# Optimization experiments

Hardware: AMD Instinct MI355X
Metric: run time of the kernel (lower is better)

Reference implementation:

```python
import jax, jax.numpy as jnp
import numpy as np

B, T, S = 4, 16384, 256
V_DIM, L_DIM, E, H = 256, 768, 1024, 8
D = E // H  # head_dim = 128
SCALE = D ** -0.5
CLAMP = 50000.0


def setup_inputs() -> dict:
    key = jax.random.key(0)
    ks = jax.random.split(key, 8)
    w = lambda k, shp: jax.random.normal(k, shp, jnp.float32) * 0.03  # ~xavier scale
    return {
        'v': jax.random.normal(ks[0], (B, T, V_DIM), jnp.float32),
        'l': jax.random.normal(ks[1], (B, S, L_DIM), jnp.float32),
        'v_proj_w': w(ks[2], (V_DIM, E)), 'v_proj_b': jnp.zeros((E,), jnp.float32),
        'l_proj_w': w(ks[3], (L_DIM, E)), 'l_proj_b': jnp.zeros((E,), jnp.float32),
        'vv_w': w(ks[4], (V_DIM, E)), 'vv_b': jnp.zeros((E,), jnp.float32),
        'vl_w': w(ks[5], (L_DIM, E)), 'vl_b': jnp.zeros((E,), jnp.float32),
        'ov_w': w(ks[6], (E, V_DIM)), 'ov_b': jnp.zeros((V_DIM,), jnp.float32),
        'ol_w': w(ks[7], (E, L_DIM)), 'ol_b': jnp.zeros((L_DIM,), jnp.float32),
    }


def _heads(x):
    # [B, N, E] -> [B, H, N, D]
    b, n, _ = x.shape
    return x.reshape(b, n, H, D).transpose(0, 2, 1, 3)


def reference(v, l, v_proj_w, v_proj_b, l_proj_w, l_proj_b,
              vv_w, vv_b, vl_w, vl_b, ov_w, ov_b, ol_w, ol_b):
    b, t, _ = v.shape
    s = l.shape[1]
    q = _heads((v @ v_proj_w + v_proj_b) * SCALE)   # [B,H,T,D]
    k = _heads(l @ l_proj_w + l_proj_b)             # [B,H,S,D]
    val_v = _heads(v @ vv_w + vv_b)                 # [B,H,T,D]
    val_l = _heads(l @ vl_w + vl_b)                 # [B,H,S,D]

    attn = jnp.einsum('bhtd,bhsd->bhts', q, k)      # shared QK^T scores
    attn = jnp.clip(attn, -CLAMP, CLAMP)

    # column-direction softmax (over vision tokens) on the transpose
    attn_T = attn.transpose(0, 1, 3, 2)             # [B,H,S,T]
    attn_l = attn_T - jnp.max(attn_T, axis=-1, keepdims=True)
    attn_l = jnp.clip(attn_l, -CLAMP, CLAMP)
    attn_l = jax.nn.softmax(attn_l, axis=-1)

    # row-direction softmax (over text tokens)
    attn_v = jax.nn.softmax(attn, axis=-1)          # [B,H,T,S]

    out_v = jnp.einsum('bhts,bhsd->bhtd', attn_v, val_l)
    out_l = jnp.einsum('bhst,bhtd->bhsd', attn_l, val_v)
    out_v = out_v.transpose(0, 2, 1, 3).reshape(b, t, E)
    out_l = out_l.transpose(0, 2, 1, 3).reshape(b, s, E)
    return out_v @ ov_w + ov_b, out_l @ ol_w + ol_b
```

## Files before the change

kernel.cpp:

```cpp
#include <hip/hip_runtime.h>
#include <hip/hip_bf16.h>
#include <hip/hip_fp16.h>

#define DI __device__ __forceinline__

typedef short bf16x8 __attribute__((ext_vector_type(8)));
typedef float f32x4 __attribute__((ext_vector_type(4)));
using bf16 = __hip_bfloat16;

typedef __attribute__((address_space(3))) void lds_void;
typedef const __attribute__((address_space(1))) void glob_void;

constexpr int Tn = 16384, Sn = 256, En = 1024;
constexpr float SCALEF = 0.08838834764831845f;
constexpr float CLAMPF = 50000.0f;

DI f32x4 mfma16(bf16x8 a, bf16x8 b, f32x4 c) {
  return __builtin_amdgcn_mfma_f32_16x16x32_bf16(a, b, c, 0, 0, 0);
}
DI unsigned short f2bu(float x) { bf16 h = __float2bfloat16(x); return *(unsigned short*)&h; }
DI unsigned int pack2(float lo, float hi) { return (unsigned)f2bu(lo) | ((unsigned)f2bu(hi) << 16); }
DI bf16x8 ldg8(const bf16* p) { return *(const bf16x8*)p; }
DI float clampf(float v) { return fminf(fmaxf(v, -CLAMPF), CLAMPF); }
DI unsigned int packh2(float a, float b) {
  __half2 h = __floats2half2_rn(a, b);
  return *(unsigned int*)&h;
}
DI void gload16(const bf16* g, bf16* lds_base) {
  __builtin_amdgcn_global_load_lds((glob_void*)g, (lds_void*)lds_base, 16, 0, 0);
}

__global__ void cast_f32_bf16_v4(const float* __restrict__ in, bf16* __restrict__ out, int n4) {
  int i = blockIdx.x * 256 + threadIdx.x;
  if (i >= n4) return;
  float4 f = reinterpret_cast<const float4*>(in)[i];
  unsigned long long u = (unsigned long long)pack2(f.x, f.y) |
                         ((unsigned long long)pack2(f.z, f.w) << 32);
  *reinterpret_cast<unsigned long long*>(out + (size_t)i * 4) = u;
}

__global__ void cast_weights(const float* __restrict__ w0, bf16* __restrict__ o0,
                             const float* __restrict__ w1, bf16* __restrict__ o1,
                             const float* __restrict__ w2, bf16* __restrict__ o2,
                             const float* __restrict__ w3, bf16* __restrict__ o3,
                             const float* __restrict__ w4, bf16* __restrict__ o4,
                             const float* __restrict__ w5, bf16* __restrict__ o5) {
  int id = blockIdx.x * 256 + threadIdx.x;
  switch (blockIdx.y) {
    case 0: if (id < 256*1024) { int k = id >> 10, n = id & 1023; o0[n*256 + k] = __float2bfloat16(w0[id]); } break;
    case 1: if (id < 256*1024) { int k = id >> 10, n = id & 1023; o1[n*256 + k] = __float2bfloat16(w1[id]); } break;
    case 2: if (id < 768*1024) { int k = id >> 10, n = id & 1023; o2[n*768 + k] = __float2bfloat16(w2[id]); } break;
    case 3: if (id < 768*1024) { int k = id >> 10, n = id & 1023; o3[n*768 + k] = __float2bfloat16(w3[id]); } break;
    case 4: if (id < 1024*256) { int k = id >> 8,  n = id & 255;  o4[n*1024 + k] = __float2bfloat16(w4[id]); } break;
    case 5: if (id < 1024*768) { int k = id / 768, n = id % 768;  o5[n*1024 + k] = __float2bfloat16(w5[id]); } break;
  }
}

template<int MODE>
__global__ __launch_bounds__(256) void gemm_kern(
    const bf16* __restrict__ A, const bf16* __restrict__ Bw0, const bf16* __restrict__ Bw1,
    const float* __restrict__ bias0, const float* __restrict__ bias1,
    void* __restrict__ out0, void* __restrict__ out1, int zbase)
{
  constexpr int K = (MODE == 0) ? 256 : (MODE == 1) ? 768 : 1024;
  const int z = blockIdx.z + zbase;
  const bf16* Bw = z ? Bw1 : Bw0;
  const float* bias = z ? bias1 : bias0;
  const int m0 = blockIdx.x * 128, n0 = blockIdx.y * 128;
  const int tid = threadIdx.x, lane = tid & 63;
  const int w = tid >> 6, wm = w >> 1, wn = w & 1;
  const int l15 = lane & 15, l4 = lane >> 4;

  __shared__ bf16 smem[128 * 136];
  bf16* As = smem;
  bf16* Bs = smem + 128 * 64;

  const int lr = lane >> 3, lp = lane & 7;

  f32x4 acc[4][4];
  #pragma unroll
  for (int a = 0; a < 4; a++)
    #pragma unroll
    for (int c = 0; c < 4; c++) acc[a][c] = f32x4{0.f, 0.f, 0.f, 0.f};

  for (int k0 = 0; k0 < K; k0 += 64) {
    __syncthreads();
    #pragma unroll
    for (int it = 0; it < 4; it++) {
      const int row = it * 32 + w * 8 + lr;
      const int gc = lp ^ (row & 7);
      gload16(Bw + (size_t)(n0 + row) * K + k0 + gc * 8, Bs + (it * 32 + w * 8) * 64);
      gload16(A  + (size_t)(m0 + row) * K + k0 + gc * 8, As + (it * 32 + w * 8) * 64);
    }
    __syncthreads();
    #pragma unroll
    for (int ks = 0; ks < 2; ks++) {
      bf16x8 af[4], bfr[4];
      #pragma unroll
      for (int mf = 0; mf < 4; mf++) {
        int r = wm * 64 + mf * 16 + l15;
        af[mf] = *(const bf16x8*)(As + r * 64 + (((ks * 4 + l4) ^ (r & 7)) * 8));
      }
      #pragma unroll
      for (int nf = 0; nf < 4; nf++) {
        int r = wn * 64 + nf * 16 + l15;
        bfr[nf] = *(const bf16x8*)(Bs + r * 64 + (((ks * 4 + l4) ^ (r & 7)) * 8));
      }
      #pragma unroll
      for (int mf = 0; mf < 4; mf++)
        #pragma unroll
        for (int nf = 0; nf < 4; nf++)
          acc[mf][nf] = mfma16(af[mf], bfr[nf], acc[mf][nf]);
    }
  }
  __syncthreads();

  if constexpr (MODE <= 1) {
    #pragma unroll
    for (int nf = 0; nf < 4; nf++) {
      int nl = wn * 64 + nf * 16 + l15;
      float bv = bias[n0 + nl];
      #pragma unroll
      for (int mf = 0; mf < 4; mf++) {
        int ml = wm * 64 + mf * 16 + l4 * 4;
        #pragma unroll
        for (int i = 0; i < 4; i++) {
          float vv = acc[mf][nf][i] + bv;
          if (MODE == 0 && z == 0) vv *= SCALEF;
          smem[(ml + i) * 136 + nl] = __float2bfloat16(vv);
        }
      }
    }
    __syncthreads();
    constexpr int TT = (MODE == 0) ? Tn : Sn;
    const int h = n0 >> 7;
    const int r2 = tid >> 1, c0 = (tid & 1) * 64;
    if (z == 0) {
      int m = m0 + r2;
      int bq = (MODE == 0) ? 0 : (m >> 8);
      int t  = m & (TT - 1);
      bf16* out = (bf16*)out0;
      size_t base = ((size_t)(bq * 8 + h) * TT + t) * 128 + c0;
      #pragma unroll
      for (int j = 0; j < 32; j++) {
        unsigned int u = *(const unsigned int*)(smem + r2 * 136 + c0 + 2 * j);
        *(unsigned int*)(out + base + 2 * j) = u;
      }
    } else {
      int bq = (MODE == 0) ? 0 : (m0 >> 8);
      int t0 = m0 & (TT - 1);
      bf16* out = (bf16*)out1;
      size_t base = ((size_t)(bq * 8 + h) * 128 + r2) * TT + t0 + c0;
      #pragma unroll
      for (int j = 0; j < 32; j++) {
        unsigned short u0 = *(const unsigned short*)(smem + (c0 + 2 * j)     * 136 + r2);
        unsigned short u1 = *(const unsigned short*)(smem + (c0 + 2 * j + 1) * 136 + r2);
        *(unsigned int*)(out + base + 2 * j) = (unsigned)u0 | ((unsigned)u1 << 16);
      }
    }
  } else {
    constexpr int NOUT = (MODE == 2) ? 256 : 768;
    float* out = (float*)out0;
    #pragma unroll
    for (int nf = 0; nf < 4; nf++) {
      int n = n0 + wn * 64 + nf * 16 + l15;
      float bv = bias[n];
      #pragma unroll
      for (int mf = 0; mf < 4; mf++) {
        size_t mbase = (size_t)(m0 + wm * 64 + mf * 16 + l4 * 4) * NOUT + n;
        #pragma unroll
        for (int i = 0; i < 4; i++)
          out[mbase + (size_t)i * NOUT] = acc[mf][nf][i] + bv;
      }
    }
  }
}

template<int NCH, bool SLAB>
__global__ __launch_bounds__(512, 2) void attn_fused(
    const bf16* __restrict__ qh,
    const bf16* __restrict__ kh,
    const bf16* __restrict__ vallT,
    const bf16* __restrict__ valvT,
    bf16* __restrict__ ovh,
    void* __restrict__ col_dst,
    float* __restrict__ dsum_dst)
{
  constexpr int SPAN = Tn / NCH;
  constexpr int TILES = SPAN / 64;
  const int ch = blockIdx.x, h = blockIdx.y;
  const int tid = threadIdx.x, lane = tid & 63, w = tid >> 6;
  const int l15 = lane & 15, l4 = lane >> 4;
  const int sw = w * 32;
  const int e7 = l15 & 7;

  __shared__ bf16 Qb[2][64 * 128];
  __shared__ bf16 Vb[2][128 * 64];
  __shared__ bf16 Enat[64 * 264];
  __shared__ bf16 Etr[8][32 * 72];
  __shared__ float red[8][64];

  const bf16* qp  = qh    + (size_t)h * Tn * 128;
  const bf16* kp  = kh    + (size_t)h * Sn * 128;
  const bf16* vlp = vallT + (size_t)h * 128 * Sn;
  const bf16* vvp = valvT + (size_t)h * 128 * Tn;
  const int tb0 = ch * SPAN;

  bf16x8 bkr[4][2];
  #pragma unroll
  for (int ks = 0; ks < 4; ks++)
    #pragma unroll
    for (int si = 0; si < 2; si++)
      bkr[ks][si] = ldg8(kp + (size_t)(sw + si * 16 + l15) * 128 + ks * 32 + l4 * 8);
  bf16x8 bvr[8];
  #pragma unroll
  for (int ks2 = 0; ks2 < 8; ks2++)
    bvr[ks2] = ldg8(vlp + (size_t)(w * 16 + l15) * Sn + ks2 * 32 + l4 * 8);

  const int q_r0 = tid >> 4, q_c = tid & 15;
  const int q_r1 = q_r0 + 32;
  const int v_r0 = tid >> 3, v_c = tid & 7;
  const int v_r1 = v_r0 + 64;

  {
    uint4 q0 = *(const uint4*)(qp + (size_t)(tb0 + q_r0) * 128 + q_c * 8);
    uint4 q1 = *(const uint4*)(qp + (size_t)(tb0 + q_r1) * 128 + q_c * 8);
    uint4 v0 = *(const uint4*)(vvp + (size_t)v_r0 * Tn + tb0 + v_c * 8);
    uint4 v1 = *(const uint4*)(vvp + (size_t)v_r1 * Tn + tb0 + v_c * 8);
    *(uint4*)(&Qb[0][q_r0 * 128 + ((q_c ^ (q_r0 & 7)) * 8)]) = q0;
    *(uint4*)(&Qb[0][q_r1 * 128 + ((q_c ^ (q_r1 & 7)) * 8)]) = q1;
    *(uint4*)(&Vb[0][v_r0 * 64  + ((v_c ^ (v_r0 & 7)) * 8)]) = v0;
    *(uint4*)(&Vb[0][v_r1 * 64  + ((v_c ^ (v_r1 & 7)) * 8)]) = v1;
  }
  __syncthreads();

  f32x4 oc[8][2];
  #pragma unroll
  for (int a = 0; a < 8; a++)
    #pragma unroll
    for (int c = 0; c < 2; c++) oc[a][c] = f32x4{0.f, 0.f, 0.f, 0.f};
  float csum[2] = {0.f, 0.f};

  int cur = 0;
  for (int tt = 0; tt < TILES; tt++) {
    const int tb = tb0 + tt * 64;
    const bool hn = (tt + 1 < TILES);
    uint4 pfq0, pfq1, pfv0, pfv1;
    if (hn) {
      const int tbn = tb + 64;
      pfq0 = *(const uint4*)(qp + (size_t)(tbn + q_r0) * 128 + q_c * 8);
      pfq1 = *(const uint4*)(qp + (size_t)(tbn + q_r1) * 128 + q_c * 8);
      pfv0 = *(const uint4*)(vvp + (size_t)v_r0 * Tn + tbn + v_c * 8);
      pfv1 = *(const uint4*)(vvp + (size_t)v_r1 * Tn + tbn + v_c * 8);
    }
    f32x4 sacc[4][2];
    #pragma unroll
    for (int a = 0; a < 4; a++)
      #pragma unroll
      for (int c = 0; c < 2; c++) sacc[a][c] = f32x4{0.f, 0.f, 0.f, 0.f};
    #pragma unroll
    for (int ks = 0; ks < 4; ks++) {
      const int x = (ks * 4 + l4) ^ e7;
      bf16x8 aq[4];
      #pragma unroll
      for (int ti = 0; ti < 4; ti++)
        aq[ti] = *(const bf16x8*)(&Qb[cur][(ti * 16 + l15) * 128 + x * 8]);
      #pragma unroll
      for (int ti = 0; ti < 4; ti++)
        #pragma unroll
        for (int si = 0; si < 2; si++)
          sacc[ti][si] = mfma16(aq[ti], bkr[ks][si], sacc[ti][si]);
    }
    float rp[4][4];
    #pragma unroll
    for (int ti = 0; ti < 4; ti++)
      #pragma unroll
      for (int i = 0; i < 4; i++) rp[ti][i] = 0.f;
    #pragma unroll
    for (int ti = 0; ti < 4; ti++)
      #pragma unroll
      for (int si = 0; si < 2; si++) {
        float e0 = __expf(clampf(sacc[ti][si][0]));
        float e1 = __expf(clampf(sacc[ti][si][1]));
        float e2 = __expf(clampf(sacc[ti][si][2]));
        float e3 = __expf(clampf(sacc[ti][si][3]));
        csum[si] += (e0 + e1) + (e2 + e3);
        rp[ti][0] += e0; rp[ti][1] += e1; rp[ti][2] += e2; rp[ti][3] += e3;
        unsigned long long u = (unsigned long long)pack2(e0, e1) |
                               ((unsigned long long)pack2(e2, e3) << 32);
        *(unsigned long long*)(&Etr[w][(si * 16 + l15) * 72 + ti * 16 + l4 * 4]) = u;
        const int s = sw + si * 16 + l15;
        const int t0 = ti * 16 + l4 * 4;
        Enat[(t0 + 0) * 264 + s] = __float2bfloat16(e0);
        Enat[(t0 + 1) * 264 + s] = __float2bfloat16(e1);
        Enat[(t0 + 2) * 264 + s] = __float2bfloat16(e2);
        Enat[(t0 + 3) * 264 + s] = __float2bfloat16(e3);
      }
    #pragma unroll
    for (int ti = 0; ti < 4; ti++)
      #pragma unroll
      for (int i = 0; i < 4; i++) {
        float r = rp[ti][i];
        #pragma unroll
        for (int off = 1; off < 16; off <<= 1) r += __shfl_xor(r, off);
        if (l15 == 0) red[w][ti * 16 + l4 * 4 + i] = r;
      }
    __syncthreads();
    float rsm[4][4];
    #pragma unroll
    for (int ti = 0; ti < 4; ti++)
      #pragma unroll
      for (int i = 0; i < 4; i++) {
        const int tl = ti * 16 + l4 * 4 + i;
        float s = red[0][tl] + red[1][tl] + red[2][tl] + red[3][tl] +
                  red[4][tl] + red[5][tl] + red[6][tl] + red[7][tl];
        rsm[ti][i] = 1.0f / s;
      }
    f32x4 orr[4];
    #pragma unroll
    for (int a = 0; a < 4; a++) orr[a] = f32x4{0.f, 0.f, 0.f, 0.f};
    #pragma unroll
    for (int ks2 = 0; ks2 < 8; ks2++) {
      const int soff = ks2 * 32 + l4 * 8;
      #pragma unroll
      for (int ti = 0; ti < 4; ti++) {
        bf16x8 ap = *(const bf16x8*)(Enat + (ti * 16 + l15) * 264 + soff);
        orr[ti] = mfma16(ap, bvr[ks2], orr[ti]);
      }
    }
    #pragma unroll
    for (int ti = 0; ti < 4; ti++) {
      size_t base = (size_t)(tb + ti * 16 + l4 * 4) * En + h * 128 + w * 16 + l15;
      #pragma unroll
      for (int i = 0; i < 4; i++)
        ovh[base + (size_t)i * En] = __float2bfloat16(orr[ti][i] * rsm[ti][i]);
    }
    #pragma unroll
    for (int kst = 0; kst < 2; kst++) {
      bf16x8 bp[2];
      #pragma unroll
      for (int si = 0; si < 2; si++)
        bp[si] = *(const bf16x8*)(&Etr[w][(si * 16 + l15) * 72 + kst * 32 + l4 * 8]);
      const int x = (kst * 4 + l4) ^ e7;
      #pragma unroll
      for (int mf = 0; mf < 8; mf++) {
        bf16x8 av = *(const bf16x8*)(&Vb[cur][(mf * 16 + l15) * 64 + x * 8]);
        #pragma unroll
        for (int si = 0; si < 2; si++)
          oc[mf][si] = mfma16(av, bp[si], oc[mf][si]);
      }
    }
    if (hn) {
      *(uint4*)(&Qb[cur ^ 1][q_r0 * 128 + ((q_c ^ (q_r0 & 7)) * 8)]) = pfq0;
      *(uint4*)(&Qb[cur ^ 1][q_r1 * 128 + ((q_c ^ (q_r1 & 7)) * 8)]) = pfq1;
      *(uint4*)(&Vb[cur ^ 1][v_r0 * 64  + ((v_c ^ (v_r0 & 7)) * 8)]) = pfv0;
      *(uint4*)(&Vb[cur ^ 1][v_r1 * 64  + ((v_c ^ (v_r1 & 7)) * 8)]) = pfv1;
    }
    __syncthreads();
    cur ^= 1;
  }
  #pragma unroll
  for (int si = 0; si < 2; si++) {
    float c = csum[si];
    c += __shfl_xor(c, 16);
    c += __shfl_xor(c, 32);
    if (l4 == 0) {
      if constexpr (SLAB) dsum_dst[((size_t)(ch * 8 + h)) * 256 + sw + si * 16 + l15] = c;
      else atomicAdd(&dsum_dst[h * 256 + sw + si * 16 + l15], c);
    }
  }
  if constexpr (SLAB) {
    __half* slab = (__half*)col_dst + ((size_t)(ch * 8 + h) * 256) * 128;
    #pragma unroll
    for (int mf = 0; mf < 8; mf++)
      #pragma unroll
      for (int si = 0; si < 2; si++) {
        const int s = sw + si * 16 + l15;
        const int d = mf * 16 + l4 * 4;
        uint2 u;
        u.x = packh2(oc[mf][si][0], oc[mf][si][1]);
        u.y = packh2(oc[mf][si][2], oc[mf][si][3]);
        *(uint2*)(slab + (size_t)s * 128 + d) = u;
      }
  } else {
    float* olh = (float*)col_dst;
    #pragma unroll
    for (int mf = 0; mf < 8; mf++)
      #pragma unroll
      for (int si = 0; si < 2; si++) {
        const int s = sw + si * 16 + l15;
        const int d = mf * 16 + l4 * 4;
        float* dst = olh + (size_t)s * 1024 + h * 128 + d;
        #pragma unroll
        for (int i = 0; i < 4; i++) atomicAdd(dst + i, oc[mf][si][i]);
      }
  }
}

template<int NCH>
__global__ __launch_bounds__(256) void reduce_olh(
    const __half* __restrict__ slab, const float* __restrict__ csum_slab, bf16* __restrict__ olhb)
{
  int id = blockIdx.x * 256 + threadIdx.x;
  int s = id >> 8, hd4 = id & 255, h = hd4 >> 5, d4 = hd4 & 31;
  float a0 = 0.f, a1 = 0.f, a2 = 0.f, a3 = 0.f, dsv = 0.f;
  #pragma unroll 4
  for (int ch = 0; ch < NCH; ch++) {
    uint2 u = *(const uint2*)(slab + ((size_t)(ch * 8 + h) * 256 + s) * 128 + d4 * 4);
    __half2 x = *(__half2*)&u.x, y = *(__half2*)&u.y;
    a0 += __low2float(x); a1 += __high2float(x);
    a2 += __low2float(y); a3 += __high2float(y);
    dsv += csum_slab[((size_t)(ch * 8 + h)) * 256 + s];
  }
  float inv = 1.0f / dsv;
  unsigned long long u = (unsigned long long)pack2(a0 * inv, a1 * inv) |
                         ((unsigned long long)pack2(a2 * inv, a3 * inv) << 32);
  *reinterpret_cast<unsigned long long*>(olhb + (size_t)s * 1024 + h * 128 + d4 * 4) = u;
}

__global__ __launch_bounds__(256) void norm_olh(
    const float* __restrict__ olh, const float* __restrict__ dsum, bf16* __restrict__ olhb)
{
  int i = blockIdx.x * 256 + threadIdx.x;
  int s = i >> 8, c4 = i & 255;
  float inv = 1.0f / dsum[(c4 >> 5) * 256 + s];
  float4 x = reinterpret_cast<const float4*>(olh + (size_t)s * 1024)[c4];
  unsigned long long u = (unsigned long long)pack2(x.x * inv, x.y * inv) |
                         ((unsigned long long)pack2(x.z * inv, x.w * inv) << 32);
  *reinterpret_cast<unsigned long long*>(olhb + (size_t)s * 1024 + c4 * 4) = u;
}

extern "C" void kernel_launch(void* const* d_in, const int* in_sizes, int n_in,
                              void* d_out, int out_size, void* d_ws, size_t ws_size,
                              hipStream_t stream)
{
  (void)in_sizes; (void)n_in;
  const float* v        = (const float*)d_in[0];
  const float* l        = (const float*)d_in[1];
  const float* v_proj_w = (const float*)d_in[2];
  const float* v_proj_b = (const float*)d_in[3];
  const float* l_proj_w = (const float*)d_in[4];
  const float* l_proj_b = (const float*)d_in[5];
  const float* vv_w     = (const float*)d_in[6];
  const float* vv_b     = (const float*)d_in[7];
  const float* vl_w     = (const float*)d_in[8];
  const float* vl_b     = (const float*)d_in[9];
  const float* ov_w     = (const float*)d_in[10];
  const float* ov_b     = (const float*)d_in[11];
  const float* ol_w     = (const float*)d_in[12];
  const float* ol_b     = (const float*)d_in[13];

  char* ws = (char*)d_ws;
  size_t off = 0;
  auto alloc = [&](size_t bytes) -> char* {
    char* p = ws + off;
    off += (bytes + 255) & ~(size_t)255;
    return p;
  };

  bf16*  wqt   = (bf16*)alloc((size_t)1024 * 256 * 2);
  bf16*  wvvt  = (bf16*)alloc((size_t)1024 * 256 * 2);
  bf16*  wkt   = (bf16*)alloc((size_t)1024 * 768 * 2);
  bf16*  wvlt  = (bf16*)alloc((size_t)1024 * 768 * 2);
  bf16*  wovt  = (bf16*)alloc((size_t)256 * 1024 * 2);
  bf16*  wolt  = (bf16*)alloc((size_t)768 * 1024 * 2);
  bf16*  lb    = (bf16*)alloc((size_t)1024 * 768 * 2);
  bf16*  kh    = (bf16*)alloc((size_t)32 * 256 * 128 * 2);
  bf16*  vallT = (bf16*)alloc((size_t)32 * 128 * 256 * 2);
  float* olh   = (float*)alloc((size_t)1024 * 1024 * 4);
  bf16*  olhb  = (bf16*)alloc((size_t)1024 * 1024 * 2);
  float* dsum  = (float*)alloc((size_t)2048 * 4);
  bf16*  vb_b    = (bf16*)alloc((size_t)16384 * 256 * 2);
  bf16*  qh_b    = (bf16*)alloc((size_t)8 * 16384 * 128 * 2);
  bf16*  valvT_b = (bf16*)alloc((size_t)8 * 128 * 16384 * 2);
  bf16*  ovh_b   = (bf16*)alloc((size_t)16384 * 1024 * 2);
  const size_t off_base = off;

  const size_t slabh_b = (size_t)32 * 8 * 256 * 128 * 2;
  const size_t csum_b  = (size_t)32 * 8 * 256 * 4;
  int tier;
  if (off_base + slabh_b + csum_b <= ws_size) tier = 0;
  else if (off_base <= ws_size) tier = 2;
  else {
    hipMemsetAsync(d_out, 0xFF, (size_t)out_size * 4, stream);
    return;
  }
  __half* slabh     = (__half*)(ws + off_base);
  float*  csum_slab = (float*)(ws + off_base + slabh_b);

  if (tier == 2) hipMemsetAsync(olh, 0, (size_t)1024 * 1024 * 4, stream);

  cast_weights<<<dim3(3072, 6), 256, 0, stream>>>(v_proj_w, wqt, vv_w, wvvt,
                                                  l_proj_w, wkt, vl_w, wvlt, ov_w, wovt, ol_w, wolt);
  cast_f32_bf16_v4<<<768, 256, 0, stream>>>(l, lb, 196608);
  gemm_kern<1><<<dim3(8, 8, 2), 256, 0, stream>>>(lb, wkt, wvlt, l_proj_b, vl_b, kh, vallT, 0);

  for (int b = 0; b < 4; b++) {
    const bf16*  kh_b    = kh    + (size_t)b * 8 * Sn * 128;
    const bf16*  vallT_b = vallT + (size_t)b * 8 * 128 * Sn;
    cast_f32_bf16_v4<<<4096, 256, 0, stream>>>(v + (size_t)b * 16384 * 256, vb_b, 1048576);
    gemm_kern<0><<<dim3(128, 8, 2), 256, 0, stream>>>(vb_b, wqt, wvvt, v_proj_b, vv_b,
                                                      qh_b, valvT_b, 0);
    if (tier == 0) {
      attn_fused<32, true><<<dim3(32, 8), 512, 0, stream>>>(qh_b, kh_b, vallT_b, valvT_b,
                                                            ovh_b, slabh, csum_slab);
    } else {
      hipMemsetAsync(dsum, 0, (size_t)2048 * 4, stream);
      attn_fused<32, false><<<dim3(32, 8), 512, 0, stream>>>(qh_b, kh_b, vallT_b, valvT_b,
                                                             ovh_b, olh + (size_t)b * 256 * 1024, dsum);
    }
    gemm_kern<2><<<dim3(128, 2, 1), 256, 0, stream>>>(ovh_b, wovt, wovt, ov_b, ov_b,
                                                      (float*)d_out + (size_t)b * 16384 * 256, nullptr, 0);
    if (tier == 0) reduce_olh<32><<<256, 256, 0, stream>>>(slabh, csum_slab, olhb + (size_t)b * 256 * 1024);
    else           norm_olh<<<256, 256, 0, stream>>>(olh + (size_t)b * 256 * 1024, dsum,
                                                     olhb + (size_t)b * 256 * 1024);
  }

  gemm_kern<3><<<dim3(8, 6, 1), 256, 0, stream>>>(olhb, wolt, wolt, ol_b, ol_b,
                                                  (float*)d_out + 16777216, nullptr, 0);
}
```

Before: 646.0 us.

## Stage out_v tile through LDS for coalesced stores and raise MFMA priority

The per-tile attention output for the vision stream is written to a swizzled shared-memory buffer. It is then stored to global memory one iteration later as 16-byte coalesced vectors, replacing the scattered 2-byte stores. MFMA sections are wrapped in s_setprio to favor matrix-issuing waves, and the symmetric score clamp is replaced by a one-sided cap before exp. This adds 16KB of LDS per block, which may reduce occupancy, and the deferred store relies on the existing end-of-loop barrier for correctness.

New measurement: 731.2 us. 1.13x slower.

```diff
diff --git a/kernel.cpp b/kernel.cpp
--- a/kernel.cpp
+++ b/kernel.cpp
@@ -13,7 +13,7 @@
 
 constexpr int Tn = 16384, Sn = 256, En = 1024;
 constexpr float SCALEF = 0.08838834764831845f;
-constexpr float CLAMPF = 50000.0f;
+constexpr float EXPCAP = 80.0f;
 
 DI f32x4 mfma16(bf16x8 a, bf16x8 b, f32x4 c) {
   return __builtin_amdgcn_mfma_f32_16x16x32_bf16(a, b, c, 0, 0, 0);
@@ -21,7 +21,6 @@
 DI unsigned short f2bu(float x) { bf16 h = __float2bfloat16(x); return *(unsigned short*)&h; }
 DI unsigned int pack2(float lo, float hi) { return (unsigned)f2bu(lo) | ((unsigned)f2bu(hi) << 16); }
 DI bf16x8 ldg8(const bf16* p) { return *(const bf16x8*)p; }
-DI float clampf(float v) { return fminf(fmaxf(v, -CLAMPF), CLAMPF); }
 DI unsigned int packh2(float a, float b) {
   __half2 h = __floats2half2_rn(a, b);
   return *(unsigned int*)&h;
@@ -198,6 +197,7 @@
   __shared__ bf16 Vb[2][128 * 64];
   __shared__ bf16 Enat[64 * 264];
   __shared__ bf16 Etr[8][32 * 72];
+  __shared__ bf16 Ob[64 * 128];
   __shared__ float red[8][64];
 
   const bf16* qp  = qh    + (size_t)h * Tn * 128;
@@ -221,6 +221,8 @@
   const int q_r1 = q_r0 + 32;
   const int v_r0 = tid >> 3, v_c = tid & 7;
   const int v_r1 = v_r0 + 64;
+  const int o_r0 = tid >> 4, o_c = tid & 15;
+  const int o_r1 = o_r0 + 32;
 
   {
     uint4 q0 = *(const uint4*)(qp + (size_t)(tb0 + q_r0) * 128 + q_c * 8);
@@ -253,11 +255,19 @@
       pfv0 = *(const uint4*)(vvp + (size_t)v_r0 * Tn + tbn + v_c * 8);
       pfv1 = *(const uint4*)(vvp + (size_t)v_r1 * Tn + tbn + v_c * 8);
     }
+    if (tt > 0) {
+      const int tbp = tb - 64;
+      uint4 o0 = *(const uint4*)(&Ob[o_r0 * 128 + ((o_c ^ (o_r0 & 7)) * 8)]);
+      uint4 o1 = *(const uint4*)(&Ob[o_r1 * 128 + ((o_c ^ (o_r1 & 7)) * 8)]);
+      *(uint4*)(ovh + (size_t)(tbp + o_r0) * En + h * 128 + o_c * 8) = o0;
+      *(uint4*)(ovh + (size_t)(tbp + o_r1) * En + h * 128 + o_c * 8) = o1;
+    }
     f32x4 sacc[4][2];
     #pragma unroll
     for (int a = 0; a < 4; a++)
       #pragma unroll
       for (int c = 0; c < 2; c++) sacc[a][c] = f32x4{0.f, 0.f, 0.f, 0.f};
+    __builtin_amdgcn_s_setprio(1);
     #pragma unroll
     for (int ks = 0; ks < 4; ks++) {
       const int x = (ks * 4 + l4) ^ e7;
@@ -271,6 +281,7 @@
         for (int si = 0; si < 2; si++)
           sacc[ti][si] = mfma16(aq[ti], bkr[ks][si], sacc[ti][si]);
     }
+    __builtin_amdgcn_s_setprio(0);
     float rp[4][4];
     #pragma unroll
     for (int ti = 0; ti < 4; ti++)
@@ -280,10 +291,10 @@
     for (int ti = 0; ti < 4; ti++)
       #pragma unroll
       for (int si = 0; si < 2; si++) {
-        float e0 = __expf(clampf(sacc[ti][si][0]));
-        float e1 = __expf(clampf(sacc[ti][si][1]));
-        float e2 = __expf(clampf(sacc[ti][si][2]));
-        float e3 = __expf(clampf(sacc[ti][si][3]));
+        float e0 = __expf(fminf(sacc[ti][si][0], EXPCAP));
+        float e1 = __expf(fminf(sacc[ti][si][1], EXPCAP));
+        float e2 = __expf(fminf(sacc[ti][si][2], EXPCAP));
+        float e3 = __expf(fminf(sacc[ti][si][3], EXPCAP));
         csum[si] += (e0 + e1) + (e2 + e3);
         rp[ti][0] += e0; rp[ti][1] += e1; rp[ti][2] += e2; rp[ti][3] += e3;
         unsigned long long u = (unsigned long long)pack2(e0, e1) |
@@ -319,6 +330,7 @@
     f32x4 orr[4];
     #pragma unroll
     for (int a = 0; a < 4; a++) orr[a] = f32x4{0.f, 0.f, 0.f, 0.f};
+    __builtin_amdgcn_s_setprio(1);
     #pragma unroll
     for (int ks2 = 0; ks2 < 8; ks2++) {
       const int soff = ks2 * 32 + l4 * 8;
@@ -328,13 +340,19 @@
         orr[ti] = mfma16(ap, bvr[ks2], orr[ti]);
       }
     }
+    __builtin_amdgcn_s_setprio(0);
     #pragma unroll
     for (int ti = 0; ti < 4; ti++) {
-      size_t base = (size_t)(tb + ti * 16 + l4 * 4) * En + h * 128 + w * 16 + l15;
-      #pragma unroll
-      for (int i = 0; i < 4; i++)
-        ovh[base + (size_t)i * En] = __float2bfloat16(orr[ti][i] * rsm[ti][i]);
-    }
+      #pragma unroll
+      for (int i = 0; i < 4; i++) {
+        const int t = ti * 16 + l4 * 4 + i;
+        const int e = w * 16 + l15;
+        const int chk = e >> 3, within = e & 7;
+        Ob[t * 128 + ((chk ^ (t & 7)) * 8) + within] =
+            __float2bfloat16(orr[ti][i] * rsm[ti][i]);
+      }
+    }
+    __builtin_amdgcn_s_setprio(1);
     #pragma unroll
     for (int kst = 0; kst < 2; kst++) {
       bf16x8 bp[2];
@@ -350,6 +368,7 @@
           oc[mf][si] = mfma16(av, bp[si], oc[mf][si]);
       }
     }
+    __builtin_amdgcn_s_setprio(0);
     if (hn) {
       *(uint4*)(&Qb[cur ^ 1][q_r0 * 128 + ((q_c ^ (q_r0 & 7)) * 8)]) = pfq0;
       *(uint4*)(&Qb[cur ^ 1][q_r1 * 128 + ((q_c ^ (q_r1 & 7)) * 8)]) = pfq1;
@@ -358,6 +377,13 @@
     }
     __syncthreads();
     cur ^= 1;
+  }
+  {
+    const int tbp = tb0 + (TILES - 1) * 64;
+    uint4 o0 = *(const uint4*)(&Ob[o_r0 * 128 + ((o_c ^ (o_r0 & 7)) * 8)]);
+    uint4 o1 = *(const uint4*)(&Ob[o_r1 * 128 + ((o_c ^ (o_r1 & 7)) * 8)]);
+    *(uint4*)(ovh + (size_t)(tbp + o_r0) * En + h * 128 + o_c * 8) = o0;
+    *(uint4*)(ovh + (size_t)(tbp + o_r1) * En + h * 128 + o_c * 8) = o1;
   }
   #pragma unroll
   for (int si = 0; si < 2; si++) {
```
